# Optimization experiments

Measured on AMD Instinct MI355X. Metric: run time of the kernel, lower is better.

## Reference

```python
import jax, jax.numpy as jnp
import numpy as np

LMAX = 3
N_NODES = 100000
C_IN = 128
C_OUT = 128
M = (LMAX + 1) ** 2  # 16 spherical components
# l index for each m component: m in [l^2, (l+1)^2) belongs to l
L_OF_M = np.array([int(np.floor(np.sqrt(m))) for m in range(M)], dtype=np.int32)


def setup_inputs() -> dict:
    key = jax.random.key(0)
    kx, kw = jax.random.split(key)
    x = jax.random.normal(kx, (N_NODES, M, C_IN), dtype=jnp.float32)
    weights = jax.random.normal(kw, (LMAX + 1, C_IN, C_OUT), dtype=jnp.float32)
    return {"x": x, "weights": weights}


def reference(x, weights):
    # x: [N, M, C_in]; weights: [L+1, C_in, C_out]
    # e3nn path_weight for a single-path linear: 1/sqrt(fan_in)
    pw = 1.0 / jnp.sqrt(jnp.asarray(C_IN, dtype=x.dtype))
    w_m = weights[jnp.asarray(L_OF_M)]  # [M, C_in, C_out] gathered per m-component
    # block-diagonal (per-l) matmul, same weight shared across the 2l+1 m's of each l
    y = jnp.einsum('nmc,mcd->nmd', x, w_m) * pw
    return y
```

## Files before the change

kernel.cpp:

```cpp
#include <hip/hip_runtime.h>


typedef __bf16 bf16x8 __attribute__((ext_vector_type(8)));
typedef float f32x4 __attribute__((ext_vector_type(4)));
typedef unsigned short u16x8 __attribute__((ext_vector_type(8)));

#define N_NODES 100000
#define MCOMP 16
#define CIN 128
#define ROWSTRIDE (MCOMP * CIN)

__device__ __forceinline__ unsigned short f2b(float f) {
    unsigned int u = __float_as_uint(f);
    unsigned int r = (u + 0x7fffu + ((u >> 16) & 1u)) >> 16;
    return (unsigned short)r;
}

__global__ void prep_weights(const float* __restrict__ w,
                             unsigned short* __restrict__ wt) {
    int idx = blockIdx.x * blockDim.x + threadIdx.x;
    int l = idx >> 14;
    int rem = idx & 16383;
    int d = rem >> 7;
    int c = rem & 127;
    const float pw = 0.08838834764831845f;
    wt[idx] = f2b(w[(l << 14) + (c << 7) + d] * pw);
}

__global__ __launch_bounds__(256, 4) void linear_mfma(
        const float* __restrict__ x,
        const unsigned short* __restrict__ wt,
        float* __restrict__ y) {
    __shared__ float lds0[32 * 128];
    __shared__ float lds1[32 * 128];

    const int m = blockIdx.x;
    const int l = (m >= 9) ? 3 : (m >= 4) ? 2 : (m >= 1) ? 1 : 0;
    const int wid = threadIdx.x >> 6;
    const int lane = threadIdx.x & 63;
    const int lr = lane & 15;
    const int lk = lane >> 4;
    const int nbase = blockIdx.y * 128;

    const unsigned short* wl = wt + (l << 14);
    bf16x8 wf[2][4];
#pragma unroll
    for (int df = 0; df < 2; ++df)
#pragma unroll
        for (int kk = 0; kk < 4; ++kk)
            wf[df][kk] = __builtin_bit_cast(bf16x8, *(const u16x8*)(
                wl + (((wid * 32 + df * 16 + lr) << 7) + kk * 32 + lk * 8)));

    auto stage = [&](float* buf, int h) {
        const int hbase = nbase + h * 32;
#pragma unroll
        for (int j = 0; j < 4; ++j) {
            int seg = wid * 4 + j;
            int row = seg * 2 + (lane >> 5);
            int slot = (lane & 31) ^ (row & 7);
            const float* src = x + (size_t)(hbase + row) * ROWSTRIDE
                               + m * CIN + slot * 4;
            __builtin_amdgcn_global_load_lds(
                (const __attribute__((address_space(1))) void*)src,
                (__attribute__((address_space(3))) void*)(buf + seg * 256),
                16, 0, 0);
        }
    };

    auto comp = [&](const float* buf, int h) {
        f32x4 acc[2][2];
#pragma unroll
        for (int rf = 0; rf < 2; ++rf)
#pragma unroll
            for (int df = 0; df < 2; ++df)
                acc[rf][df] = (f32x4){0.f, 0.f, 0.f, 0.f};

#pragma unroll
        for (int kk = 0; kk < 4; ++kk) {
#pragma unroll
            for (int rf = 0; rf < 2; ++rf) {
                int row = rf * 16 + lr;
                int sw = row & 7;
                const float* rbase = buf + row * 128 + kk * 32;
                f32x4 v0 = *(const f32x4*)(rbase + ((lk * 2) ^ sw) * 4);
                f32x4 v1 = *(const f32x4*)(rbase + ((lk * 2 + 1) ^ sw) * 4);
                bf16x8 xb;
#pragma unroll
                for (int jj = 0; jj < 4; ++jj) {
                    xb[jj] = (__bf16)v0[jj];
                    xb[jj + 4] = (__bf16)v1[jj];
                }
                acc[rf][0] = __builtin_amdgcn_mfma_f32_16x16x32_bf16(
                    wf[0][kk], xb, acc[rf][0], 0, 0, 0);
                acc[rf][1] = __builtin_amdgcn_mfma_f32_16x16x32_bf16(
                    wf[1][kk], xb, acc[rf][1], 0, 0, 0);
            }
        }
        const int hbase = nbase + h * 32;
#pragma unroll
        for (int rf = 0; rf < 2; ++rf)
#pragma unroll
            for (int df = 0; df < 2; ++df) {
                float* yp = y + (size_t)(hbase + rf * 16 + lr) * ROWSTRIDE
                            + m * CIN + wid * 32 + df * 16 + lk * 4;
                *(f32x4*)yp = acc[rf][df];
            }
    };

    if (nbase + 128 <= N_NODES) {
        stage(lds0, 0);
        asm volatile("s_waitcnt vmcnt(0)" ::: "memory");
        __builtin_amdgcn_s_barrier();

        stage(lds1, 1);
        __builtin_amdgcn_sched_barrier(0);
        comp(lds0, 0);
        asm volatile("s_waitcnt vmcnt(4)" ::: "memory");
        __builtin_amdgcn_s_barrier();

        stage(lds0, 2);
        __builtin_amdgcn_sched_barrier(0);
        comp(lds1, 1);
        asm volatile("s_waitcnt vmcnt(4)" ::: "memory");
        __builtin_amdgcn_s_barrier();

        stage(lds1, 3);
        __builtin_amdgcn_sched_barrier(0);
        comp(lds0, 2);
        asm volatile("s_waitcnt vmcnt(4)" ::: "memory");
        __builtin_amdgcn_s_barrier();

        comp(lds1, 3);
    } else {
        stage(lds0, 0);
        asm volatile("s_waitcnt vmcnt(0)" ::: "memory");
        __builtin_amdgcn_s_barrier();
        comp(lds0, 0);
    }
}

extern "C" void kernel_launch(void* const* d_in, const int* in_sizes, int n_in,
                              void* d_out, int out_size, void* d_ws, size_t ws_size,
                              hipStream_t stream) {
    const float* x = (const float*)d_in[0];
    const float* w = (const float*)d_in[1];
    float* y = (float*)d_out;
    unsigned short* wt = (unsigned short*)d_ws;

    prep_weights<<<256, 256, 0, stream>>>(w, wt);

    dim3 grid(MCOMP, (N_NODES + 127) / 128);
    linear_mfma<<<grid, 256, 0, stream>>>(x, wt, y);
}
```

Before: 309.3 us.

## Process two spherical components per block with 16-row stages

Each block now covers two adjacent m components and 16 node rows per stage instead of one component and 32 rows. Each row's staged load becomes one contiguous 1 KB segment, and the LDS swizzle and fragment indexing are reworked to match. The aim is better-coalesced global loads and stores on a kernel limited by memory bandwidth. In exchange, each block keeps weight fragments for both components in registers, which doubles that register use, and the tail block runs a two-stage path.

```diff
diff --git a/kernel.cpp b/kernel.cpp
--- a/kernel.cpp
+++ b/kernel.cpp
@@ -9,6 +9,7 @@
 #define MCOMP 16
 #define CIN 128
 #define ROWSTRIDE (MCOMP * CIN)
+#define TROWS 16
 
 __device__ __forceinline__ unsigned short f2b(float f) {
     unsigned int u = __float_as_uint(f);
@@ -31,38 +32,41 @@
         const float* __restrict__ x,
         const unsigned short* __restrict__ wt,
         float* __restrict__ y) {
-    __shared__ float lds0[32 * 128];
-    __shared__ float lds1[32 * 128];
+    __shared__ float lds0[TROWS * 256];
+    __shared__ float lds1[TROWS * 256];
 
-    const int m = blockIdx.x;
-    const int l = (m >= 9) ? 3 : (m >= 4) ? 2 : (m >= 1) ? 1 : 0;
+    const int m0 = blockIdx.x * 2;
     const int wid = threadIdx.x >> 6;
     const int lane = threadIdx.x & 63;
     const int lr = lane & 15;
     const int lk = lane >> 4;
-    const int nbase = blockIdx.y * 128;
+    const int nbase = blockIdx.y * (4 * TROWS);
 
-    const unsigned short* wl = wt + (l << 14);
-    bf16x8 wf[2][4];
+    bf16x8 wf[2][2][4];
 #pragma unroll
-    for (int df = 0; df < 2; ++df)
+    for (int mu = 0; mu < 2; ++mu) {
+        int m = m0 + mu;
+        int l = (m >= 9) ? 3 : (m >= 4) ? 2 : (m >= 1) ? 1 : 0;
+        const unsigned short* wl = wt + (l << 14);
 #pragma unroll
-        for (int kk = 0; kk < 4; ++kk)
-            wf[df][kk] = __builtin_bit_cast(bf16x8, *(const u16x8*)(
-                wl + (((wid * 32 + df * 16 + lr) << 7) + kk * 32 + lk * 8)));
+        for (int df = 0; df < 2; ++df)
+#pragma unroll
+            for (int kk = 0; kk < 4; ++kk)
+                wf[mu][df][kk] = __builtin_bit_cast(bf16x8, *(const u16x8*)(
+                    wl + (((wid * 32 + df * 16 + lr) << 7) + kk * 32 + lk * 8)));
+    }
 
     auto stage = [&](float* buf, int h) {
-        const int hbase = nbase + h * 32;
+        const int hbase = nbase + h * TROWS;
 #pragma unroll
         for (int j = 0; j < 4; ++j) {
-            int seg = wid * 4 + j;
-            int row = seg * 2 + (lane >> 5);
-            int slot = (lane & 31) ^ (row & 7);
-            const float* src = x + (size_t)(hbase + row) * ROWSTRIDE
-                               + m * CIN + slot * 4;
+            int r = wid * 4 + j;
+            int slot = lane ^ (r & 7);
+            const float* src = x + (size_t)(hbase + r) * ROWSTRIDE
+                               + m0 * CIN + slot * 4;
             __builtin_amdgcn_global_load_lds(
                 (const __attribute__((address_space(1))) void*)src,
-                (__attribute__((address_space(3))) void*)(buf + seg * 256),
+                (__attribute__((address_space(3))) void*)(buf + r * 256),
                 16, 0, 0);
         }
     };
@@ -70,44 +74,45 @@
     auto comp = [&](const float* buf, int h) {
         f32x4 acc[2][2];
 #pragma unroll
-        for (int rf = 0; rf < 2; ++rf)
+        for (int mu = 0; mu < 2; ++mu)
 #pragma unroll
             for (int df = 0; df < 2; ++df)
-                acc[rf][df] = (f32x4){0.f, 0.f, 0.f, 0.f};
+                acc[mu][df] = (f32x4){0.f, 0.f, 0.f, 0.f};
 
 #pragma unroll
-        for (int kk = 0; kk < 4; ++kk) {
+        for (int kk = 0; kk < 4; ++kk)
 #pragma unroll
-            for (int rf = 0; rf < 2; ++rf) {
-                int row = rf * 16 + lr;
-                int sw = row & 7;
-                const float* rbase = buf + row * 128 + kk * 32;
-                f32x4 v0 = *(const f32x4*)(rbase + ((lk * 2) ^ sw) * 4);
-                f32x4 v1 = *(const f32x4*)(rbase + ((lk * 2 + 1) ^ sw) * 4);
+            for (int mu = 0; mu < 2; ++mu) {
+                const int sw = lr & 7;
+                const float* rbase = buf + lr * 256;
+                int s0 = (mu * 32 + kk * 8 + lk * 2) ^ sw;
+                int s1 = (mu * 32 + kk * 8 + lk * 2 + 1) ^ sw;
+                f32x4 v0 = *(const f32x4*)(rbase + s0 * 4);
+                f32x4 v1 = *(const f32x4*)(rbase + s1 * 4);
                 bf16x8 xb;
 #pragma unroll
                 for (int jj = 0; jj < 4; ++jj) {
                     xb[jj] = (__bf16)v0[jj];
                     xb[jj + 4] = (__bf16)v1[jj];
                 }
-                acc[rf][0] = __builtin_amdgcn_mfma_f32_16x16x32_bf16(
-                    wf[0][kk], xb, acc[rf][0], 0, 0, 0);
-                acc[rf][1] = __builtin_amdgcn_mfma_f32_16x16x32_bf16(
-                    wf[1][kk], xb, acc[rf][1], 0, 0, 0);
+                acc[mu][0] = __builtin_amdgcn_mfma_f32_16x16x32_bf16(
+                    wf[mu][0][kk], xb, acc[mu][0], 0, 0, 0);
+                acc[mu][1] = __builtin_amdgcn_mfma_f32_16x16x32_bf16(
+                    wf[mu][1][kk], xb, acc[mu][1], 0, 0, 0);
             }
-        }
-        const int hbase = nbase + h * 32;
+
+        const int hbase = nbase + h * TROWS;
 #pragma unroll
-        for (int rf = 0; rf < 2; ++rf)
+        for (int mu = 0; mu < 2; ++mu)
 #pragma unroll
             for (int df = 0; df < 2; ++df) {
-                float* yp = y + (size_t)(hbase + rf * 16 + lr) * ROWSTRIDE
-                            + m * CIN + wid * 32 + df * 16 + lk * 4;
-                *(f32x4*)yp = acc[rf][df];
+                float* yp = y + (size_t)(hbase + lr) * ROWSTRIDE
+                            + (m0 + mu) * CIN + wid * 32 + df * 16 + lk * 4;
+                *(f32x4*)yp = acc[mu][df];
             }
     };
 
-    if (nbase + 128 <= N_NODES) {
+    if (nbase + 4 * TROWS <= N_NODES) {
         stage(lds0, 0);
         asm volatile("s_waitcnt vmcnt(0)" ::: "memory");
         __builtin_amdgcn_s_barrier();
@@ -133,9 +138,13 @@
         comp(lds1, 3);
     } else {
         stage(lds0, 0);
-        asm volatile("s_waitcnt vmcnt(0)" ::: "memory");
+        stage(lds1, 1);
+        asm volatile("s_waitcnt vmcnt(4)" ::: "memory");
         __builtin_amdgcn_s_barrier();
         comp(lds0, 0);
+        asm volatile("s_waitcnt vmcnt(4)" ::: "memory");
+        __builtin_amdgcn_s_barrier();
+        comp(lds1, 1);
     }
 }
 
@@ -149,6 +158,6 @@
 
     prep_weights<<<256, 256, 0, stream>>>(w, wt);
 
-    dim3 grid(MCOMP, (N_NODES + 127) / 128);
+    dim3 grid(MCOMP / 2, (N_NODES + 4 * TROWS - 1) / (4 * TROWS));
     linear_mfma<<<grid, 256, 0, stream>>>(x, wt, y);
 }
```

Result: slower. 602.6 us (+94.8%).

## Process two m-components per block with 512 threads for wider contiguous loads

Applied to the files above, without the earlier changes.

Each block now handles two adjacent spherical components (m0, m0+1) with 8 waves, four per component, so every staged row read covers 1 KB of contiguous x instead of 512 bytes. LDS tiles double to 32x256 floats, and the grid halves along m. The aim is better DRAM access efficiency and fewer blocks. The cost is double the LDS per block (64 KB), which may limit occupancy, and a 512-thread launch bound that could add register pressure.

```diff
diff --git a/kernel.cpp b/kernel.cpp
--- a/kernel.cpp
+++ b/kernel.cpp
@@ -9,6 +9,8 @@
 #define MCOMP 16
 #define CIN 128
 #define ROWSTRIDE (MCOMP * CIN)
+#define TROWS 32
+#define TPB 4
 
 __device__ __forceinline__ unsigned short f2b(float f) {
     unsigned int u = __float_as_uint(f);
@@ -27,20 +29,24 @@
     wt[idx] = f2b(w[(l << 14) + (c << 7) + d] * pw);
 }
 
-__global__ __launch_bounds__(256, 4) void linear_mfma(
+__global__ __launch_bounds__(512, 4) void linear_mfma(
         const float* __restrict__ x,
         const unsigned short* __restrict__ wt,
         float* __restrict__ y) {
-    __shared__ float lds0[32 * 128];
-    __shared__ float lds1[32 * 128];
+    __shared__ float lds0[TROWS * 256];
+    __shared__ float lds1[TROWS * 256];
 
-    const int m = blockIdx.x;
-    const int l = (m >= 9) ? 3 : (m >= 4) ? 2 : (m >= 1) ? 1 : 0;
+    const int m0 = blockIdx.x * 2;
     const int wid = threadIdx.x >> 6;
+    const int mu = wid >> 2;
+    const int wq = wid & 3;
     const int lane = threadIdx.x & 63;
     const int lr = lane & 15;
     const int lk = lane >> 4;
-    const int nbase = blockIdx.y * 128;
+    const int nbase = blockIdx.y * (TROWS * TPB);
+
+    const int m = m0 + mu;
+    const int l = (m >= 9) ? 3 : (m >= 4) ? 2 : (m >= 1) ? 1 : 0;
 
     const unsigned short* wl = wt + (l << 14);
     bf16x8 wf[2][4];
@@ -49,25 +55,24 @@
 #pragma unroll
         for (int kk = 0; kk < 4; ++kk)
             wf[df][kk] = __builtin_bit_cast(bf16x8, *(const u16x8*)(
-                wl + (((wid * 32 + df * 16 + lr) << 7) + kk * 32 + lk * 8)));
+                wl + (((wq * 32 + df * 16 + lr) << 7) + kk * 32 + lk * 8)));
 
-    auto stage = [&](float* buf, int h) {
-        const int hbase = nbase + h * 32;
+    auto stage = [&](float* buf, int t) {
+        const int hbase = nbase + t * TROWS;
 #pragma unroll
         for (int j = 0; j < 4; ++j) {
-            int seg = wid * 4 + j;
-            int row = seg * 2 + (lane >> 5);
-            int slot = (lane & 31) ^ (row & 7);
-            const float* src = x + (size_t)(hbase + row) * ROWSTRIDE
-                               + m * CIN + slot * 4;
+            int r = wid * 4 + j;
+            int slot = lane ^ (r & 7);
+            const float* src = x + (size_t)(hbase + r) * ROWSTRIDE
+                               + m0 * CIN + slot * 4;
             __builtin_amdgcn_global_load_lds(
                 (const __attribute__((address_space(1))) void*)src,
-                (__attribute__((address_space(3))) void*)(buf + seg * 256),
+                (__attribute__((address_space(3))) void*)(buf + r * 256),
                 16, 0, 0);
         }
     };
 
-    auto comp = [&](const float* buf, int h) {
+    auto comp = [&](const float* buf, int t) {
         f32x4 acc[2][2];
 #pragma unroll
         for (int rf = 0; rf < 2; ++rf)
@@ -76,12 +81,12 @@
                 acc[rf][df] = (f32x4){0.f, 0.f, 0.f, 0.f};
 
 #pragma unroll
-        for (int kk = 0; kk < 4; ++kk) {
+        for (int kk = 0; kk < 4; ++kk)
 #pragma unroll
             for (int rf = 0; rf < 2; ++rf) {
                 int row = rf * 16 + lr;
                 int sw = row & 7;
-                const float* rbase = buf + row * 128 + kk * 32;
+                const float* rbase = buf + row * 256 + mu * 128 + kk * 32;
                 f32x4 v0 = *(const f32x4*)(rbase + ((lk * 2) ^ sw) * 4);
                 f32x4 v1 = *(const f32x4*)(rbase + ((lk * 2 + 1) ^ sw) * 4);
                 bf16x8 xb;
@@ -95,19 +100,19 @@
                 acc[rf][1] = __builtin_amdgcn_mfma_f32_16x16x32_bf16(
                     wf[1][kk], xb, acc[rf][1], 0, 0, 0);
             }
-        }
-        const int hbase = nbase + h * 32;
+
+        const int hbase = nbase + t * TROWS;
 #pragma unroll
         for (int rf = 0; rf < 2; ++rf)
 #pragma unroll
             for (int df = 0; df < 2; ++df) {
                 float* yp = y + (size_t)(hbase + rf * 16 + lr) * ROWSTRIDE
-                            + m * CIN + wid * 32 + df * 16 + lk * 4;
+                            + m * CIN + wq * 32 + df * 16 + lk * 4;
                 *(f32x4*)yp = acc[rf][df];
             }
     };
 
-    if (nbase + 128 <= N_NODES) {
+    if (nbase + TROWS * TPB <= N_NODES) {
         stage(lds0, 0);
         asm volatile("s_waitcnt vmcnt(0)" ::: "memory");
         __builtin_amdgcn_s_barrier();
@@ -149,6 +154,6 @@
 
     prep_weights<<<256, 256, 0, stream>>>(w, wt);
 
-    dim3 grid(MCOMP, (N_NODES + 127) / 128);
-    linear_mfma<<<grid, 256, 0, stream>>>(x, wt, y);
+    dim3 grid(MCOMP / 2, (N_NODES + TROWS * TPB - 1) / (TROWS * TPB));
+    linear_mfma<<<grid, 512, 0, stream>>>(x, wt, y);
 }
```

Result: no change. 304.8 us (median of 2 runs) (-1.4%).
